# Kernel optimization log

Measured on AMD Instinct MI355X. Metric: run time of the kernel, lower is better.

## Reference

```python
import jax, jax.numpy as jnp
import numpy as np

B, S, D, H, BS, L, FF, V = 2, 4096, 1024, 16, 64, 4, 4096, 50000
HD = D // H; NB = S // BS; NM = NB - 2; R = 3

def layernorm(x, g, b):
    mu = x.mean(-1, keepdims=True)
    var = ((x - mu) ** 2).mean(-1, keepdims=True)
    return (x - mu) * jax.lax.rsqrt(var + 1e-5) * g + b

def bigbird_attn(x, neg, rand_attn, Wq, bq, Wk, bk, Wv, bv, Wo, bo):
    heads = lambda t: t.reshape(B, S, H, HD).transpose(0, 2, 1, 3)
    q, k, v = heads(x @ Wq + bq), heads(x @ Wk + bk), heads(x @ Wv + bv)
    scale = np.float32(1.0 / np.sqrt(HD))
    qb = q.reshape(B, H, NB, BS, HD); kb = k.reshape(B, H, NB, BS, HD); vb = v.reshape(B, H, NB, BS, HD)
    negb = neg.reshape(B, NB, BS)
    # global query blocks (first & last) attend densely to all keys
    qg = jnp.concatenate([qb[:, :, 0], qb[:, :, -1]], axis=2)  # [B,H,2*BS,HD]
    sg = jnp.einsum('bhqd,bhkd->bhqk', qg, k) * scale + neg[:, None, None, :]
    ctx_g = jnp.einsum('bhqk,bhkd->bhqd', jax.nn.softmax(sg, -1), v)
    # middle query blocks: sliding window(3) + global(2) + random(R) key blocks
    win_k = jnp.stack([kb[:, :, i:i + NM] for i in range(3)], axis=3)  # [B,H,NM,3,BS,HD]
    win_v = jnp.stack([vb[:, :, i:i + NM] for i in range(3)], axis=3)
    gidx = jnp.array([0, NB - 1])
    g_k = jnp.broadcast_to(kb[:, :, gidx][:, :, None], (B, H, NM, 2, BS, HD))
    g_v = jnp.broadcast_to(vb[:, :, gidx][:, :, None], (B, H, NM, 2, BS, HD))
    hix = jnp.arange(H)[:, None, None]
    r_k = kb[:, hix, rand_attn]  # [B,H,NM,R,BS,HD]
    r_v = vb[:, hix, rand_attn]
    K = 3 + 2 + R
    keys = jnp.concatenate([win_k, g_k, r_k], axis=3).reshape(B, H, NM, K * BS, HD)
    vals = jnp.concatenate([win_v, g_v, r_v], axis=3).reshape(B, H, NM, K * BS, HD)
    win_m = jnp.stack([negb[:, i:i + NM] for i in range(3)], axis=2)  # [B,NM,3,BS]
    g_m = jnp.broadcast_to(negb[:, gidx][:, None], (B, NM, 2, BS))
    m_wg = jnp.concatenate([win_m, g_m], axis=2).reshape(B, 1, NM, 5 * BS)
    r_m = negb[:, rand_attn].reshape(B, H, NM, R * BS)
    m_all = jnp.concatenate([jnp.broadcast_to(m_wg, (B, H, NM, 5 * BS)), r_m], axis=-1)
    sm = jnp.einsum('bhnqd,bhnkd->bhnqk', qb[:, :, 1:-1], keys) * scale + m_all[:, :, :, None, :]
    ctx_m = jnp.einsum('bhnqk,bhnkd->bhnqd', jax.nn.softmax(sm, -1), vals)
    ctx = jnp.concatenate([ctx_g[:, :, None, :BS], ctx_m, ctx_g[:, :, None, BS:]], axis=2)
    out = ctx.reshape(B, H, S, HD).transpose(0, 2, 1, 3).reshape(B, S, D)
    return out @ Wo + bo

def reference(input_ids, attention_mask, rand_attn, emb, Wq, bq, Wk, bk, Wv, bv, Wo, bo, ln1_g, ln1_b, W1, b1, W2, b2, ln2_g, ln2_b, lnf_g, lnf_b, projW, projb):
    x = emb[input_ids]
    neg = (1.0 - attention_mask.astype(jnp.float32)) * (-1e9)
    for l in range(L):  # pre-norm transformer encoder layers
        x = x + bigbird_attn(layernorm(x, ln1_g[l], ln1_b[l]), neg, rand_attn,
                             Wq[l], bq[l], Wk[l], bk[l], Wv[l], bv[l], Wo[l], bo[l])
        h = layernorm(x, ln2_g[l], ln2_b[l])
        x = x + (jax.nn.gelu(h @ W1[l] + b1[l]) @ W2[l] + b2[l])
    x = layernorm(x, lnf_g, lnf_b)
    feats = x.mean(axis=1)  # pooled output (mean over tokens)
    feats = feats / jnp.maximum(jnp.linalg.norm(feats, axis=-1, keepdims=True), 1e-12)
    return feats @ projW + projb

def setup_inputs():
    key = jax.random.key(0)
    ks = jax.random.split(key, 16)
    init = lambda k, shp: (0.02 * jax.random.normal(k, shp)).astype(jnp.float32)
    return {
        'input_ids': jax.random.randint(ks[0], (B, S), 0, V),
        'attention_mask': jnp.ones((B, S), dtype=jnp.int32),
        'rand_attn': jax.random.randint(ks[1], (H, NM, R), 1, NB - 1),
        'emb': init(ks[2], (V, D)),
        'Wq': init(ks[3], (L, D, D)), 'bq': jnp.zeros((L, D), jnp.float32),
        'Wk': init(ks[4], (L, D, D)), 'bk': jnp.zeros((L, D), jnp.float32),
        'Wv': init(ks[5], (L, D, D)), 'bv': jnp.zeros((L, D), jnp.float32),
        'Wo': init(ks[6], (L, D, D)), 'bo': jnp.zeros((L, D), jnp.float32),
        'ln1_g': jnp.ones((L, D), jnp.float32), 'ln1_b': jnp.zeros((L, D), jnp.float32),
        'W1': init(ks[7], (L, D, FF)), 'b1': jnp.zeros((L, FF), jnp.float32),
        'W2': init(ks[8], (L, FF, D)), 'b2': jnp.zeros((L, D), jnp.float32),
        'ln2_g': jnp.ones((L, D), jnp.float32), 'ln2_b': jnp.zeros((L, D), jnp.float32),
        'lnf_g': jnp.ones((D,), jnp.float32), 'lnf_b': jnp.zeros((D,), jnp.float32),
        'projW': init(ks[9], (D, 512)), 'projb': jnp.zeros((512,), jnp.float32),
    }
```

## Files before the change

kernel.cpp:

```cpp
#include <hip/hip_runtime.h>
#include <hip/hip_bf16.h>
#include <cstdint>
#include <cstddef>

#define BATCH 2
#define SEQ   4096
#define DIM   1024
#define NHEAD 16
#define HDIM  64
#define NBLK  64
#define NMID  62
#define NRAND 3
#define NLAYER 4
#define FFDIM 4096
#define ROWS  (BATCH*SEQ)
#define KSPL  8
#define QKVLD (3*DIM)

using f32x4 = __attribute__((ext_vector_type(4))) float;
using s16x8 = __attribute__((ext_vector_type(8))) short;
using s16x4 = __attribute__((ext_vector_type(4))) short;

__device__ inline float bf2f(short s) {
    unsigned u = ((unsigned)(unsigned short)s) << 16;
    union { unsigned u; float f; } cv; cv.u = u; return cv.f;
}
__device__ inline short f2bf(float f) {
    union { float f; unsigned u; } cv; cv.f = f;
    unsigned u = cv.u;
    unsigned r = (u + 0x7fffu + ((u >> 16) & 1u)) >> 16;
    return (short)r;
}
__device__ inline float gelu_f(float x) {
    float u = 0.7978845608028654f * (x + 0.044715f * x * x * x);
    return 0.5f * x * (1.f + tanhf(u));
}

__device__ inline void gload16(const short* g, short* l) {
    __builtin_amdgcn_global_load_lds(
        (const __attribute__((address_space(1))) void*)g,
        (__attribute__((address_space(3))) void*)l,
        16, 0, 0);
}

__global__ __launch_bounds__(256) void embed_kernel(
    const int* __restrict__ ids, const float* __restrict__ emb, float* __restrict__ x)
{
    int row = blockIdx.x;
    int id  = ids[row];
    ((float4*)x)[(size_t)row * 256 + threadIdx.x] =
        ((const float4*)emb)[(size_t)id * 256 + threadIdx.x];
}

__global__ __launch_bounds__(256) void neg_kernel(
    const int* __restrict__ mask, float* __restrict__ neg)
{
    int i = blockIdx.x * 256 + threadIdx.x;
    if (i < ROWS) neg[i] = (1.f - (float)mask[i]) * -1e9f;
}

__global__ __launch_bounds__(256) void biaspack_kernel(
    const float* __restrict__ bq, const float* __restrict__ bk,
    const float* __restrict__ bv, float* __restrict__ b3)
{
    int i = blockIdx.x * 256 + threadIdx.x;
    float v = (i < DIM) ? bq[i] : (i < 2 * DIM) ? bk[i - DIM] : bv[i - 2 * DIM];
    b3[i] = v;
}

template<int OUTBF>
__global__ __launch_bounds__(256) void ln_kernel(
    const float* __restrict__ x, const float* __restrict__ g,
    const float* __restrict__ bia, void* __restrict__ out)
{
    __shared__ float s1[4], s2[4];
    int row = blockIdx.x, t = threadIdx.x;
    const float* xr = x + (size_t)row * DIM;
    float4 v = ((const float4*)xr)[t];
    float s = v.x + v.y + v.z + v.w;
    #pragma unroll
    for (int o = 32; o > 0; o >>= 1) s += __shfl_xor(s, o, 64);
    if ((t & 63) == 0) s1[t >> 6] = s;
    __syncthreads();
    float mu = (s1[0] + s1[1] + s1[2] + s1[3]) * (1.f / DIM);
    float dx = v.x - mu, dy = v.y - mu, dz = v.z - mu, dw = v.w - mu;
    float q = dx*dx + dy*dy + dz*dz + dw*dw;
    #pragma unroll
    for (int o = 32; o > 0; o >>= 1) q += __shfl_xor(q, o, 64);
    if ((t & 63) == 0) s2[t >> 6] = q;
    __syncthreads();
    float var = (s2[0] + s2[1] + s2[2] + s2[3]) * (1.f / DIM);
    float rs  = rsqrtf(var + 1e-5f);
    float4 gg = ((const float4*)g)[t];
    float4 bb = ((const float4*)bia)[t];
    float o0 = dx * rs * gg.x + bb.x;
    float o1 = dy * rs * gg.y + bb.y;
    float o2 = dz * rs * gg.z + bb.z;
    float o3 = dw * rs * gg.w + bb.w;
    if (OUTBF) {
        s16x4 ov = { f2bf(o0), f2bf(o1), f2bf(o2), f2bf(o3) };
        ((s16x4*)out)[(size_t)row * (DIM/4) + t] = ov;
    } else {
        float4 ov = { o0, o1, o2, o3 };
        ((float4*)out)[(size_t)row * (DIM/4) + t] = ov;
    }
}

__global__ __launch_bounds__(256) void wconv_kernel(
    const float* __restrict__ W, short* __restrict__ Wt, int K, int N)
{
    __shared__ float tile[32][33];
    int k0 = blockIdx.x * 32, n0 = blockIdx.y * 32;
    int t = threadIdx.x;
    int r = t >> 3, c = (t & 7) * 4;
    float4 v = *(const float4*)(W + (size_t)(k0 + r) * N + n0 + c);
    tile[r][c+0] = v.x; tile[r][c+1] = v.y; tile[r][c+2] = v.z; tile[r][c+3] = v.w;
    __syncthreads();
    s16x4 ov;
    #pragma unroll
    for (int jj = 0; jj < 4; ++jj) ov[jj] = f2bf(tile[c + jj][r]);
    *(s16x4*)(Wt + (size_t)(n0 + r) * K + k0 + c) = ov;
}

__global__ __launch_bounds__(256) void vtrans_kernel(
    const short* __restrict__ qkv, short* __restrict__ vT)
{
    __shared__ short tile[64][66];
    const int sb = blockIdx.x, h = blockIdx.y, b = blockIdx.z;
    const int t = threadIdx.x;
    {
        int row = t >> 2, c0 = (t & 3) * 16;
        const short* src = qkv + 2 * DIM + (size_t)(b * SEQ + sb * 64 + row) * QKVLD + h * HDIM + c0;
        s16x8 a0 = ((const s16x8*)src)[0];
        s16x8 a1 = ((const s16x8*)src)[1];
        #pragma unroll
        for (int i = 0; i < 8; ++i) { tile[row][c0 + i] = a0[i]; tile[row][c0 + 8 + i] = a1[i]; }
    }
    __syncthreads();
    {
        int d = t >> 2, k0 = (t & 3) * 16;
        s16x8 o0, o1;
        #pragma unroll
        for (int i = 0; i < 8; ++i) { o0[i] = tile[k0 + i][d]; o1[i] = tile[k0 + 8 + i][d]; }
        short* dst = vT + (size_t)((b * NHEAD + h) * HDIM + d) * SEQ + sb * 64 + k0;
        ((s16x8*)dst)[0] = o0;
        ((s16x8*)dst)[1] = o1;
    }
}

template<int EPI>
__global__ __launch_bounds__(256) void gemm_kernel(
    const short* __restrict__ A, const short* __restrict__ Bt,
    const float* __restrict__ bias, const float* __restrict__ resid,
    void* __restrict__ Cout, int M, int N, int K)
{
    __shared__ short As[128 * 64];
    __shared__ short Bs[128 * 64];
    const int t = threadIdx.x;
    const int m0 = blockIdx.x * 128, n0 = blockIdx.y * 128;
    const int lane = t & 63, wave = t >> 6;
    const int wr = (wave >> 1) * 64, wc = (wave & 1) * 64;
    const int lrow = lane >> 3;
    const int lk   = (lane & 7) * 8;

    f32x4 acc[4][4];
    #pragma unroll
    for (int m = 0; m < 4; ++m)
        #pragma unroll
        for (int n = 0; n < 4; ++n)
            acc[m][n] = f32x4{0.f, 0.f, 0.f, 0.f};

    for (int kt = 0; kt < K; kt += 64) {
        #pragma unroll
        for (int c = 0; c < 4; ++c) {
            int chunk = wave * 4 + c;
            int row = chunk * 8 + lrow;
            gload16(A  + (size_t)(m0 + row) * K + kt + lk, As + chunk * 512);
            gload16(Bt + (size_t)(n0 + row) * K + kt + lk, Bs + chunk * 512);
        }
        __syncthreads();
        #pragma unroll
        for (int kk = 0; kk < 2; ++kk) {
            s16x8 af[4], bfr[4];
            #pragma unroll
            for (int i = 0; i < 4; ++i) {
                int rA = wr + i * 16 + (lane & 15);
                af[i]  = *(const s16x8*)(As + rA * 64 + kk * 32 + (lane >> 4) * 8);
                int rB = wc + i * 16 + (lane & 15);
                bfr[i] = *(const s16x8*)(Bs + rB * 64 + kk * 32 + (lane >> 4) * 8);
            }
            #pragma unroll
            for (int m = 0; m < 4; ++m)
                #pragma unroll
                for (int n = 0; n < 4; ++n)
                    acc[m][n] = __builtin_amdgcn_mfma_f32_16x16x32_bf16(
                        af[m], bfr[n], acc[m][n], 0, 0, 0);
        }
        __syncthreads();
    }

    const int rbase = m0 + wr + ((lane >> 4) << 2);
    const int cbase = n0 + wc + (lane & 15);
    #pragma unroll
    for (int m = 0; m < 4; ++m) {
        #pragma unroll
        for (int n = 0; n < 4; ++n) {
            #pragma unroll
            for (int j = 0; j < 4; ++j) {
                int row = rbase + m * 16 + j;
                int col = cbase + n * 16;
                float val = acc[m][n][j] + bias[col];
                size_t idx = (size_t)row * N + col;
                if (EPI == 1) val = gelu_f(val);
                if (EPI == 2) ((float*)Cout)[idx] = val + resid[idx];
                else          ((short*)Cout)[idx] = f2bf(val);
            }
        }
    }
}


__device__ inline void attn_tile_mfma(
    const short* __restrict__ kglob,
    const short* __restrict__ vtglob,
    const float* __restrict__ negp,
    int kld,
    short* Ks, short* Vs, float* kmask,
    const s16x8* qfrag, f32x4* o, float& mr, float& lsum)
{
    const int t = threadIdx.x;
    const int lane = t & 63;
    const int q15 = lane & 15, g = lane >> 4;
    const int sw = (lane & 7) << 4;

    {
        int row = t >> 2, c0 = (t & 3) * 16;
        int rsw = (row & 7) << 4;
        const short* ksrc = kglob + (size_t)row * kld + c0;
        s16x8 a0 = ((const s16x8*)ksrc)[0];
        s16x8 a1 = ((const s16x8*)ksrc)[1];
        char* kdst = (char*)Ks + row * 128;
        *(s16x8*)(kdst + ((c0 * 2)      ^ rsw)) = a0;
        *(s16x8*)(kdst + ((c0 * 2 + 16) ^ rsw)) = a1;
        const short* vsrc = vtglob + (size_t)row * SEQ + c0;
        s16x8 b0 = ((const s16x8*)vsrc)[0];
        s16x8 b1 = ((const s16x8*)vsrc)[1];
        char* vdst = (char*)Vs + row * 128;
        *(s16x8*)(vdst + ((c0 * 2)      ^ rsw)) = b0;
        *(s16x8*)(vdst + ((c0 * 2 + 16) ^ rsw)) = b1;
        if (t < 16) ((float4*)kmask)[t] = ((const float4*)negp)[t];
    }
    __syncthreads();

    f32x4 s[4];
    #pragma unroll
    for (int f = 0; f < 4; ++f) s[f] = f32x4{0.f, 0.f, 0.f, 0.f};
    #pragma unroll
    for (int ch = 0; ch < 2; ++ch) {
        #pragma unroll
        for (int f = 0; f < 4; ++f) {
            s16x8 kf = *(const s16x8*)((const char*)Ks + (16 * f + q15) * 128 + ((ch * 64 + g * 16) ^ sw));
            s[f] = __builtin_amdgcn_mfma_f32_16x16x32_bf16(kf, qfrag[ch], s[f], 0, 0, 0);
        }
    }

    float p[4][4];
    float mt = -1e30f;
    #pragma unroll
    for (int f = 0; f < 4; ++f) {
        float4 km = ((const float4*)kmask)[f * 4 + g];
        #pragma unroll
        for (int j = 0; j < 4; ++j) {
            float val = s[f][j] * 0.125f + ((const float*)&km)[j];
            p[f][j] = val;
            mt = fmaxf(mt, val);
        }
    }
    mt = fmaxf(mt, __shfl_xor(mt, 16, 64));
    mt = fmaxf(mt, __shfl_xor(mt, 32, 64));
    float mn = fmaxf(mr, mt);
    float psum = 0.f;
    #pragma unroll
    for (int f = 0; f < 4; ++f)
        #pragma unroll
        for (int j = 0; j < 4; ++j) {
            float e = __expf(p[f][j] - mn);
            p[f][j] = e;
            psum += e;
        }
    psum += __shfl_xor(psum, 16, 64);
    psum += __shfl_xor(psum, 32, 64);
    float fc = __expf(mr - mn);
    mr = mn;
    lsum = lsum * fc + psum;
    #pragma unroll
    for (int dt = 0; dt < 4; ++dt)
        #pragma unroll
        for (int j = 0; j < 4; ++j) o[dt][j] *= fc;

    unsigned pk[4][2];
    #pragma unroll
    for (int f = 0; f < 4; ++f)
        #pragma unroll
        for (int pp = 0; pp < 2; ++pp)
            pk[f][pp] = ((unsigned)(unsigned short)f2bf(p[f][2 * pp + 1]) << 16)
                      |  (unsigned)(unsigned short)f2bf(p[f][2 * pp]);

    const int bsel = (lane >> 4) & 1, asel = (lane >> 5) & 1;
    #pragma unroll
    for (int c = 0; c < 2; ++c) {
        union { s16x8 v; int u[4]; } pb;
        #pragma unroll
        for (int w = 0; w < 4; ++w) {
            int src = q15 + 16 * (2 * bsel + (w >> 1));
            int lo = __shfl((int)pk[2 * c][w & 1], src, 64);
            int hi = __shfl((int)pk[2 * c + 1][w & 1], src, 64);
            pb.u[w] = asel ? hi : lo;
        }
        #pragma unroll
        for (int dt = 0; dt < 4; ++dt) {
            s16x8 vf = *(const s16x8*)((const char*)Vs + (16 * dt + q15) * 128 + ((c * 64 + g * 16) ^ sw));
            o[dt] = __builtin_amdgcn_mfma_f32_16x16x32_bf16(vf, pb.v, o[dt], 0, 0, 0);
        }
    }
    __syncthreads();
}

__device__ inline void stage_q64_swz(const short* __restrict__ qglob, int qld, short* Qs)
{
    int t = threadIdx.x;
    int row = t >> 2, c0 = (t & 3) * 16;
    int rsw = (row & 7) << 4;
    const short* src = qglob + (size_t)row * qld + c0;
    s16x8 a0 = ((const s16x8*)src)[0];
    s16x8 a1 = ((const s16x8*)src)[1];
    char* dst = (char*)Qs + row * 128;
    *(s16x8*)(dst + ((c0 * 2)      ^ rsw)) = a0;
    *(s16x8*)(dst + ((c0 * 2 + 16) ^ rsw)) = a1;
}

__global__ __launch_bounds__(256) void attn_middle_mfma(
    const short* __restrict__ qkv, const short* __restrict__ vT,
    const float* __restrict__ neg, const int* __restrict__ rand_attn, short* __restrict__ ctx)
{
    __shared__ short Qs[64 * 64];
    __shared__ short Ks[64 * 64];
    __shared__ short Vs[64 * 64];
    __shared__ float kmask[64];

    const int j = blockIdx.x, h = blockIdx.y, b = blockIdx.z;
    const int n = j + 1;
    const int t = threadIdx.x;
    const int lane = t & 63, wave = t >> 6;
    const int q15 = lane & 15, g = lane >> 4;
    const int sw = (lane & 7) << 4;

    stage_q64_swz(qkv + (size_t)(b * SEQ + n * 64) * QKVLD + h * HDIM, QKVLD, Qs);
    __syncthreads();

    s16x8 qfrag[2];
    {
        int qrow = wave * 16 + q15;
        #pragma unroll
        for (int ch = 0; ch < 2; ++ch)
            qfrag[ch] = *(const s16x8*)((const char*)Qs + qrow * 128 + ((ch * 64 + g * 16) ^ sw));
    }

    int kbl[8];
    kbl[0] = n - 1; kbl[1] = n; kbl[2] = n + 1; kbl[3] = 0; kbl[4] = NBLK - 1;
    {
        const int* ra = rand_attn + ((size_t)h * NMID + j) * NRAND;
        kbl[5] = ra[0]; kbl[6] = ra[1]; kbl[7] = ra[2];
    }

    f32x4 o[4];
    #pragma unroll
    for (int dt = 0; dt < 4; ++dt) o[dt] = f32x4{0.f, 0.f, 0.f, 0.f};
    float mr = -1e30f, lsum = 0.f;

    const short* kbase  = qkv + DIM + (size_t)b * SEQ * QKVLD + h * HDIM;
    const short* vtbase = vT + (size_t)(b * NHEAD + h) * HDIM * SEQ;
    const float* negb   = neg + (size_t)b * SEQ;

    #pragma unroll 1
    for (int ib = 0; ib < 8; ++ib) {
        int kbn = kbl[ib];
        attn_tile_mfma(kbase + (size_t)kbn * 64 * QKVLD, vtbase + kbn * 64,
                       negb + kbn * 64, QKVLD, Ks, Vs, kmask, qfrag, o, mr, lsum);
    }

    float inv = 1.f / lsum;
    short* obase = ctx + (size_t)(b * SEQ + n * 64 + wave * 16 + q15) * DIM + h * HDIM;
    #pragma unroll
    for (int dt = 0; dt < 4; ++dt) {
        s16x4 ov;
        #pragma unroll
        for (int jj = 0; jj < 4; ++jj) ov[jj] = f2bf(o[dt][jj] * inv);
        *(s16x4*)(obase + dt * 16 + g * 4) = ov;
    }
}

__global__ __launch_bounds__(256) void attn_global_mfma(
    const short* __restrict__ qkv, const short* __restrict__ vT,
    const float* __restrict__ neg, float* __restrict__ part)
{
    __shared__ short Qs[64 * 64];
    __shared__ short Ks[64 * 64];
    __shared__ short Vs[64 * 64];
    __shared__ float kmask[64];

    const int qb = blockIdx.x >> 3, ks = blockIdx.x & 7;
    const int h = blockIdx.y, b = blockIdx.z;
    const int tok0 = qb ? (SEQ - 64) : 0;
    const int t = threadIdx.x;
    const int lane = t & 63, wave = t >> 6;
    const int q15 = lane & 15, g = lane >> 4;
    const int sw = (lane & 7) << 4;

    stage_q64_swz(qkv + (size_t)(b * SEQ + tok0) * QKVLD + h * HDIM, QKVLD, Qs);
    __syncthreads();

    s16x8 qfrag[2];
    {
        int qrow = wave * 16 + q15;
        #pragma unroll
        for (int ch = 0; ch < 2; ++ch)
            qfrag[ch] = *(const s16x8*)((const char*)Qs + qrow * 128 + ((ch * 64 + g * 16) ^ sw));
    }

    f32x4 o[4];
    #pragma unroll
    for (int dt = 0; dt < 4; ++dt) o[dt] = f32x4{0.f, 0.f, 0.f, 0.f};
    float mr = -1e30f, lsum = 0.f;

    const short* kbase  = qkv + DIM + (size_t)b * SEQ * QKVLD + h * HDIM;
    const short* vtbase = vT + (size_t)(b * NHEAD + h) * HDIM * SEQ;
    const float* negb   = neg + (size_t)b * SEQ;

    #pragma unroll 1
    for (int ib = 0; ib < 8; ++ib) {
        int kbn = ks * 8 + ib;
        attn_tile_mfma(kbase + (size_t)kbn * 64 * QKVLD, vtbase + kbn * 64,
                       negb + kbn * 64, QKVLD, Ks, Vs, kmask, qfrag, o, mr, lsum);
    }

    float* pbase = part + ((size_t)(((b * NHEAD + h) * 2 + qb) * KSPL + ks)) * 4224;
    int qrow = wave * 16 + q15;
    #pragma unroll
    for (int dt = 0; dt < 4; ++dt)
        *(f32x4*)(pbase + qrow * 64 + dt * 16 + g * 4) = o[dt];
    if (g == 0) { pbase[4096 + qrow] = mr; pbase[4160 + qrow] = lsum; }
}

__global__ __launch_bounds__(256) void attn_greduce(
    const float* __restrict__ part, short* __restrict__ ctx)
{
    const int qb = blockIdx.x, h = blockIdx.y, b = blockIdx.z;
    const int tok0 = qb ? (SEQ - 64) : 0;
    const int t = threadIdx.x;
    const int qq = t >> 2, d0 = (t & 3) * 16;
    const float* base = part + ((size_t)(((b * NHEAD + h) * 2 + qb) * KSPL)) * 4224;

    float m = -1e30f;
    #pragma unroll 1
    for (int s = 0; s < KSPL; ++s)
        m = fmaxf(m, base[(size_t)s * 4224 + 4096 + qq]);
    float L = 0.f;
    float acc[16];
    #pragma unroll
    for (int i = 0; i < 16; ++i) acc[i] = 0.f;
    #pragma unroll 1
    for (int s = 0; s < KSPL; ++s) {
        const float* bp = base + (size_t)s * 4224;
        float w = __expf(bp[4096 + qq] - m);
        L += w * bp[4160 + qq];
        const float4* row = (const float4*)(bp + qq * 64 + d0);
        #pragma unroll
        for (int v4 = 0; v4 < 4; ++v4) {
            float4 val = row[v4];
            acc[v4 * 4 + 0] = fmaf(w, val.x, acc[v4 * 4 + 0]);
            acc[v4 * 4 + 1] = fmaf(w, val.y, acc[v4 * 4 + 1]);
            acc[v4 * 4 + 2] = fmaf(w, val.z, acc[v4 * 4 + 2]);
            acc[v4 * 4 + 3] = fmaf(w, val.w, acc[v4 * 4 + 3]);
        }
    }
    float inv = 1.f / L;
    short* dst = ctx + (size_t)(b * SEQ + tok0 + qq) * DIM + h * HDIM + d0;
    s16x8 o0, o1;
    #pragma unroll
    for (int i = 0; i < 8; ++i) { o0[i] = f2bf(acc[i] * inv); o1[i] = f2bf(acc[8 + i] * inv); }
    ((s16x8*)dst)[0] = o0;
    ((s16x8*)dst)[1] = o1;
}

__global__ __launch_bounds__(256) void colsum1_kernel(
    const float* __restrict__ xln, float* __restrict__ partial)
{
    const int ch = blockIdx.x, b = blockIdx.y, t = threadIdx.x;
    const float* base = xln + ((size_t)b * SEQ + ch * 32) * DIM + t * 4;
    float4 acc = {0.f, 0.f, 0.f, 0.f};
    #pragma unroll 4
    for (int r = 0; r < 32; ++r) {
        float4 v = *(const float4*)(base + (size_t)r * DIM);
        acc.x += v.x; acc.y += v.y; acc.z += v.z; acc.w += v.w;
    }
    *(float4*)(partial + ((size_t)(b * 128 + ch)) * DIM + t * 4) = acc;
}

__global__ __launch_bounds__(256) void colsum2_kernel(
    const float* __restrict__ partial, float* __restrict__ feats)
{
    const int b = blockIdx.x, t = threadIdx.x;
    float4 acc = {0.f, 0.f, 0.f, 0.f};
    #pragma unroll 1
    for (int ch = 0; ch < 128; ++ch) {
        float4 v = *(const float4*)(partial + ((size_t)(b * 128 + ch)) * DIM + t * 4);
        acc.x += v.x; acc.y += v.y; acc.z += v.z; acc.w += v.w;
    }
    const float is = 1.f / SEQ;
    float4 o = { acc.x * is, acc.y * is, acc.z * is, acc.w * is };
    *(float4*)(feats + (size_t)b * DIM + t * 4) = o;
}

__global__ __launch_bounds__(256) void head_kernel(
    const float* __restrict__ feats, const float* __restrict__ projW,
    const float* __restrict__ projb, float* __restrict__ out)
{
    __shared__ float f[DIM];
    __shared__ float slots[4];
    int b = blockIdx.x, t = threadIdx.x;
    float ss = 0.f;
    for (int i = t; i < DIM; i += 256) {
        float vv = feats[b * DIM + i];
        f[i] = vv;
        ss += vv * vv;
    }
    #pragma unroll
    for (int o = 32; o > 0; o >>= 1) ss += __shfl_xor(ss, o, 64);
    if ((t & 63) == 0) slots[t >> 6] = ss;
    __syncthreads();
    float nrm = sqrtf(slots[0] + slots[1] + slots[2] + slots[3]);
    float inv = 1.f / fmaxf(nrm, 1e-12f);
    for (int o = t; o < 512; o += 256) {
        float acc = 0.f;
        for (int d = 0; d < DIM; ++d)
            acc = fmaf(f[d], projW[(size_t)d * 512 + o], acc);
        out[b * 512 + o] = acc * inv + projb[o];
    }
}

extern "C" void kernel_launch(void* const* d_in, const int* in_sizes, int n_in,
                              void* d_out, int out_size, void* d_ws, size_t ws_size,
                              hipStream_t stream)
{
    (void)in_sizes; (void)n_in; (void)out_size; (void)ws_size;
    const int*   ids   = (const int*)d_in[0];
    const int*   amask = (const int*)d_in[1];
    const int*   rnd   = (const int*)d_in[2];
    const float* emb   = (const float*)d_in[3];
    const float* Wq    = (const float*)d_in[4];
    const float* bq    = (const float*)d_in[5];
    const float* Wk    = (const float*)d_in[6];
    const float* bk    = (const float*)d_in[7];
    const float* Wv    = (const float*)d_in[8];
    const float* bv    = (const float*)d_in[9];
    const float* Wo    = (const float*)d_in[10];
    const float* bo    = (const float*)d_in[11];
    const float* ln1g  = (const float*)d_in[12];
    const float* ln1b  = (const float*)d_in[13];
    const float* W1    = (const float*)d_in[14];
    const float* b1    = (const float*)d_in[15];
    const float* W2    = (const float*)d_in[16];
    const float* b2    = (const float*)d_in[17];
    const float* ln2g  = (const float*)d_in[18];
    const float* ln2b  = (const float*)d_in[19];
    const float* lnfg  = (const float*)d_in[20];
    const float* lnfb  = (const float*)d_in[21];
    const float* projW = (const float*)d_in[22];
    const float* projb = (const float*)d_in[23];
    float* out = (float*)d_out;

    char* ws = (char*)d_ws;
    size_t off = 0;
    float* x    = (float*)(ws + off); off += (size_t)ROWS * DIM * 4;
    float* xn_f = (float*)(ws + off);
    short* xn_b = (short*)(ws + off); off += (size_t)ROWS * DIM * 4;
    short* qkv  = (short*)(ws + off); off += (size_t)ROWS * QKVLD * 2;
    short* vT   = (short*)(ws + off); off += (size_t)ROWS * DIM * 2;
    short* ctxb = (short*)(ws + off); off += (size_t)ROWS * DIM * 2;
    short* ffb  = (short*)(ws + off); off += (size_t)ROWS * FFDIM * 2;
    short* wt   = (short*)(ws + off); off += (size_t)FFDIM * DIM * 2;
    float* neg  = (float*)(ws + off); off += (size_t)ROWS * 4;
    float* bias3= (float*)(ws + off); off += (size_t)QKVLD * 4;
    float* feats= (float*)(ws + off); off += (size_t)BATCH * DIM * 4;
    float* part = (float*)(ws + off); off += (size_t)BATCH * NHEAD * 2 * KSPL * 4224 * 4;
    float* cpart= (float*)(ws + off); off += (size_t)BATCH * 128 * DIM * 4;

    embed_kernel<<<ROWS, 256, 0, stream>>>(ids, emb, x);
    neg_kernel<<<(ROWS + 255) / 256, 256, 0, stream>>>(amask, neg);

    for (int l = 0; l < NLAYER; ++l) {
        ln_kernel<1><<<ROWS, 256, 0, stream>>>(x, ln1g + l * DIM, ln1b + l * DIM, xn_b);

        wconv_kernel<<<dim3(DIM/32, DIM/32), 256, 0, stream>>>(Wq + (size_t)l*DIM*DIM, wt,                 DIM, DIM);
        wconv_kernel<<<dim3(DIM/32, DIM/32), 256, 0, stream>>>(Wk + (size_t)l*DIM*DIM, wt + 1024*1024,     DIM, DIM);
        wconv_kernel<<<dim3(DIM/32, DIM/32), 256, 0, stream>>>(Wv + (size_t)l*DIM*DIM, wt + 2*1024*1024,   DIM, DIM);
        biaspack_kernel<<<QKVLD/256, 256, 0, stream>>>(bq + l*DIM, bk + l*DIM, bv + l*DIM, bias3);
        gemm_kernel<0><<<dim3(ROWS/128, QKVLD/128), 256, 0, stream>>>(xn_b, wt, bias3, nullptr, qkv, ROWS, QKVLD, DIM);

        vtrans_kernel<<<dim3(SEQ/64, NHEAD, BATCH), 256, 0, stream>>>(qkv, vT);

        attn_global_mfma<<<dim3(2 * KSPL, NHEAD, BATCH), 256, 0, stream>>>(qkv, vT, neg, part);
        attn_middle_mfma<<<dim3(NMID, NHEAD, BATCH), 256, 0, stream>>>(qkv, vT, neg, rnd, ctxb);
        attn_greduce<<<dim3(2, NHEAD, BATCH), 256, 0, stream>>>(part, ctxb);

        wconv_kernel<<<dim3(DIM/32, DIM/32), 256, 0, stream>>>(Wo + (size_t)l*DIM*DIM, wt, DIM, DIM);
        gemm_kernel<2><<<dim3(ROWS/128, DIM/128), 256, 0, stream>>>(ctxb, wt, bo + l*DIM, x, x, ROWS, DIM, DIM);

        ln_kernel<1><<<ROWS, 256, 0, stream>>>(x, ln2g + l * DIM, ln2b + l * DIM, xn_b);

        wconv_kernel<<<dim3(DIM/32, FFDIM/32), 256, 0, stream>>>(W1 + (size_t)l*DIM*FFDIM, wt, DIM, FFDIM);
        gemm_kernel<1><<<dim3(ROWS/128, FFDIM/128), 256, 0, stream>>>(xn_b, wt, b1 + l*FFDIM, nullptr, ffb, ROWS, FFDIM, DIM);
        wconv_kernel<<<dim3(FFDIM/32, DIM/32), 256, 0, stream>>>(W2 + (size_t)l*FFDIM*DIM, wt, FFDIM, DIM);
        gemm_kernel<2><<<dim3(ROWS/128, DIM/128), 256, 0, stream>>>(ffb, wt, b2 + l*DIM, x, x, ROWS, DIM, FFDIM);
    }

    ln_kernel<0><<<ROWS, 256, 0, stream>>>(x, lnfg, lnfb, xn_f);
    colsum1_kernel<<<dim3(SEQ/32, BATCH), 256, 0, stream>>>(xn_f, cpart);
    colsum2_kernel<<<BATCH, 256, 0, stream>>>(cpart, feats);
    head_kernel<<<BATCH, 256, 0, stream>>>(feats, projW, projb, out);
}
```

Baseline: 2.037 ms.

## Swizzle GEMM LDS layout and split-K the FF2 GEMM with reduction kernel

XOR-swizzles the 16-byte chunks of each LDS tile row in the GEMM, on both the global-to-LDS write and the fragment read, to cut bank conflicts. It also adds an explicit vmcnt wait before the barrier. The FF2 GEMM (K=4096, only 512 blocks) is split into two K halves via blockIdx.z, writing fp32 partials into the reused qkv buffer. A new reduction kernel then adds the partials, bias and residual, raising parallelism at the cost of extra partial-sum memory traffic.

```diff
diff --git a/kernel.cpp b/kernel.cpp
--- a/kernel.cpp
+++ b/kernel.cpp
@@ -152,7 +152,7 @@
 __global__ __launch_bounds__(256) void gemm_kernel(
     const short* __restrict__ A, const short* __restrict__ Bt,
     const float* __restrict__ bias, const float* __restrict__ resid,
-    void* __restrict__ Cout, int M, int N, int K)
+    void* __restrict__ Cout, int M, int N, int K, int klen)
 {
     __shared__ short As[128 * 64];
     __shared__ short Bs[128 * 64];
@@ -161,7 +161,7 @@
     const int lane = t & 63, wave = t >> 6;
     const int wr = (wave >> 1) * 64, wc = (wave & 1) * 64;
     const int lrow = lane >> 3;
-    const int lk   = (lane & 7) * 8;
+    const int lksw = ((lane & 7) ^ lrow) * 8;
 
     f32x4 acc[4][4];
     #pragma unroll
@@ -170,24 +170,27 @@
         for (int n = 0; n < 4; ++n)
             acc[m][n] = f32x4{0.f, 0.f, 0.f, 0.f};
 
-    for (int kt = 0; kt < K; kt += 64) {
+    const int k0 = blockIdx.z * klen;
+    for (int kt = k0; kt < k0 + klen; kt += 64) {
         #pragma unroll
         for (int c = 0; c < 4; ++c) {
             int chunk = wave * 4 + c;
             int row = chunk * 8 + lrow;
-            gload16(A  + (size_t)(m0 + row) * K + kt + lk, As + chunk * 512);
-            gload16(Bt + (size_t)(n0 + row) * K + kt + lk, Bs + chunk * 512);
-        }
+            gload16(A  + (size_t)(m0 + row) * K + kt + lksw, As + chunk * 512);
+            gload16(Bt + (size_t)(n0 + row) * K + kt + lksw, Bs + chunk * 512);
+        }
+        asm volatile("s_waitcnt vmcnt(0)" ::: "memory");
         __syncthreads();
         #pragma unroll
         for (int kk = 0; kk < 2; ++kk) {
             s16x8 af[4], bfr[4];
+            int cb = kk * 64 + (lane >> 4) * 16;
             #pragma unroll
             for (int i = 0; i < 4; ++i) {
                 int rA = wr + i * 16 + (lane & 15);
-                af[i]  = *(const s16x8*)(As + rA * 64 + kk * 32 + (lane >> 4) * 8);
+                af[i]  = *(const s16x8*)((const char*)As + rA * 128 + (cb ^ ((rA & 7) << 4)));
                 int rB = wc + i * 16 + (lane & 15);
-                bfr[i] = *(const s16x8*)(Bs + rB * 64 + kk * 32 + (lane >> 4) * 8);
+                bfr[i] = *(const s16x8*)((const char*)Bs + rB * 128 + (cb ^ ((rB & 7) << 4)));
             }
             #pragma unroll
             for (int m = 0; m < 4; ++m)
@@ -209,14 +212,35 @@
             for (int j = 0; j < 4; ++j) {
                 int row = rbase + m * 16 + j;
                 int col = cbase + n * 16;
-                float val = acc[m][n][j] + bias[col];
                 size_t idx = (size_t)row * N + col;
-                if (EPI == 1) val = gelu_f(val);
-                if (EPI == 2) ((float*)Cout)[idx] = val + resid[idx];
-                else          ((short*)Cout)[idx] = f2bf(val);
+                float val = acc[m][n][j];
+                if (EPI == 3) {
+                    ((float*)Cout)[(size_t)blockIdx.z * ((size_t)M * N) + idx] = val;
+                } else {
+                    val += bias[col];
+                    if (EPI == 1) val = gelu_f(val);
+                    if (EPI == 2) ((float*)Cout)[idx] = val + resid[idx];
+                    else          ((short*)Cout)[idx] = f2bf(val);
+                }
             }
         }
     }
+}
+
+__global__ __launch_bounds__(256) void kred_kernel(
+    const float* __restrict__ part, const float* __restrict__ bias, float* __restrict__ x)
+{
+    const size_t MN = (size_t)ROWS * DIM;
+    size_t idx = (size_t)blockIdx.x * DIM + threadIdx.x * 4;
+    float4 p0 = *(const float4*)(part + idx);
+    float4 p1 = *(const float4*)(part + MN + idx);
+    float4 bb = *(const float4*)(bias + threadIdx.x * 4);
+    float4 xv = *(const float4*)(x + idx);
+    float4 o = { xv.x + p0.x + p1.x + bb.x,
+                 xv.y + p0.y + p1.y + bb.y,
+                 xv.z + p0.z + p1.z + bb.z,
+                 xv.w + p0.w + p1.w + bb.w };
+    *(float4*)(x + idx) = o;
 }
 
 
@@ -595,6 +619,7 @@
     float* feats= (float*)(ws + off); off += (size_t)BATCH * DIM * 4;
     float* part = (float*)(ws + off); off += (size_t)BATCH * NHEAD * 2 * KSPL * 4224 * 4;
     float* cpart= (float*)(ws + off); off += (size_t)BATCH * 128 * DIM * 4;
+    float* ff2p = (float*)qkv;
 
     embed_kernel<<<ROWS, 256, 0, stream>>>(ids, emb, x);
     neg_kernel<<<(ROWS + 255) / 256, 256, 0, stream>>>(amask, neg);
@@ -602,11 +627,11 @@
     for (int l = 0; l < NLAYER; ++l) {
         ln_kernel<1><<<ROWS, 256, 0, stream>>>(x, ln1g + l * DIM, ln1b + l * DIM, xn_b);
 
-        wconv_kernel<<<dim3(DIM/32, DIM/32), 256, 0, stream>>>(Wq + (size_t)l*DIM*DIM, wt,                 DIM, DIM);
-        wconv_kernel<<<dim3(DIM/32, DIM/32), 256, 0, stream>>>(Wk + (size_t)l*DIM*DIM, wt + 1024*1024,     DIM, DIM);
-        wconv_kernel<<<dim3(DIM/32, DIM/32), 256, 0, stream>>>(Wv + (size_t)l*DIM*DIM, wt + 2*1024*1024,   DIM, DIM);
+        wconv_kernel<<<dim3(DIM/32, DIM/32), 256, 0, stream>>>(Wq + (size_t)l*DIM*DIM, wt,               DIM, DIM);
+        wconv_kernel<<<dim3(DIM/32, DIM/32), 256, 0, stream>>>(Wk + (size_t)l*DIM*DIM, wt + 1024*1024,   DIM, DIM);
+        wconv_kernel<<<dim3(DIM/32, DIM/32), 256, 0, stream>>>(Wv + (size_t)l*DIM*DIM, wt + 2*1024*1024, DIM, DIM);
         biaspack_kernel<<<QKVLD/256, 256, 0, stream>>>(bq + l*DIM, bk + l*DIM, bv + l*DIM, bias3);
-        gemm_kernel<0><<<dim3(ROWS/128, QKVLD/128), 256, 0, stream>>>(xn_b, wt, bias3, nullptr, qkv, ROWS, QKVLD, DIM);
+        gemm_kernel<0><<<dim3(ROWS/128, QKVLD/128), 256, 0, stream>>>(xn_b, wt, bias3, nullptr, qkv, ROWS, QKVLD, DIM, DIM);
 
         vtrans_kernel<<<dim3(SEQ/64, NHEAD, BATCH), 256, 0, stream>>>(qkv, vT);
 
@@ -615,14 +640,15 @@
         attn_greduce<<<dim3(2, NHEAD, BATCH), 256, 0, stream>>>(part, ctxb);
 
         wconv_kernel<<<dim3(DIM/32, DIM/32), 256, 0, stream>>>(Wo + (size_t)l*DIM*DIM, wt, DIM, DIM);
-        gemm_kernel<2><<<dim3(ROWS/128, DIM/128), 256, 0, stream>>>(ctxb, wt, bo + l*DIM, x, x, ROWS, DIM, DIM);
+        gemm_kernel<2><<<dim3(ROWS/128, DIM/128), 256, 0, stream>>>(ctxb, wt, bo + l*DIM, x, x, ROWS, DIM, DIM, DIM);
 
         ln_kernel<1><<<ROWS, 256, 0, stream>>>(x, ln2g + l * DIM, ln2b + l * DIM, xn_b);
 
         wconv_kernel<<<dim3(DIM/32, FFDIM/32), 256, 0, stream>>>(W1 + (size_t)l*DIM*FFDIM, wt, DIM, FFDIM);
-        gemm_kernel<1><<<dim3(ROWS/128, FFDIM/128), 256, 0, stream>>>(xn_b, wt, b1 + l*FFDIM, nullptr, ffb, ROWS, FFDIM, DIM);
+        gemm_kernel<1><<<dim3(ROWS/128, FFDIM/128), 256, 0, stream>>>(xn_b, wt, b1 + l*FFDIM, nullptr, ffb, ROWS, FFDIM, DIM, DIM);
         wconv_kernel<<<dim3(FFDIM/32, DIM/32), 256, 0, stream>>>(W2 + (size_t)l*FFDIM*DIM, wt, FFDIM, DIM);
-        gemm_kernel<2><<<dim3(ROWS/128, DIM/128), 256, 0, stream>>>(ffb, wt, b2 + l*DIM, x, x, ROWS, DIM, FFDIM);
+        gemm_kernel<3><<<dim3(ROWS/128, DIM/128, 2), 256, 0, stream>>>(ffb, wt, nullptr, nullptr, ff2p, ROWS, DIM, FFDIM, FFDIM/2);
+        kred_kernel<<<ROWS, 256, 0, stream>>>(ff2p, b2 + l*DIM, x);
     }
 
     ln_kernel<0><<<ROWS, 256, 0, stream>>>(x, lnfg, lnfb, xn_f);
```

New measurement: 1.863 ms. -8.5%, faster.
